# Kernel tuning notes

Hardware: AMD Instinct MI355X
Metric: run time of the kernel (lower is better)

## Reference

```python
import jax, jax.numpy as jnp
import numpy as np

B, L1, L2, DIN, H, DK, DV = 16, 1024, 1024, 1024, 16, 64, 64


def setup_inputs() -> dict:
    key = jax.random.key(0)
    ks = jax.random.split(key, 9)
    s = 1.0 / np.sqrt(DIN)
    return {
        "x": jax.random.normal(ks[0], (B, L1, DIN), dtype=jnp.float32),
        "y": jax.random.normal(ks[1], (B, L2, DIN), dtype=jnp.float32),
        "y_mask": jax.random.randint(ks[2], (B, L2), 0, 2) == 1,  # True => masked
        "Wq": jax.random.normal(ks[3], (DIN, H * DK), dtype=jnp.float32) * s,
        "bq": jnp.zeros((H * DK,), dtype=jnp.float32),
        "Wk": jax.random.normal(ks[4], (DIN, H * DK), dtype=jnp.float32) * s,
        "bk": jnp.zeros((H * DK,), dtype=jnp.float32),
        "Wv": jax.random.normal(ks[5], (DIN, H * DV), dtype=jnp.float32) * s,
        "bv": jnp.zeros((H * DV,), dtype=jnp.float32),
    }


def reference(x, y, y_mask, Wq, bq, Wk, bk, Wv, bv):
    b, l1, _ = x.shape
    l2 = y.shape[1]
    # QKV projections, split into heads: [b, len, H, d]
    q = (x @ Wq + bq).reshape(b, l1, H, DK)
    k = (y @ Wk + bk).reshape(b, l2, H, DK)
    v = (y @ Wv + bv).reshape(b, l2, H, DV)
    # (do_relu=False -> no relu)
    scores = jnp.einsum("bqhd,bkhd->bhqk", q, k) / jnp.sqrt(jnp.float32(DK))
    scores = jnp.where(y_mask[:, None, None, :], -jnp.inf, scores)
    alpha = jax.nn.softmax(scores, axis=-1)  # over len2
    out = jnp.einsum("bhqk,bkhd->bqhd", alpha, v)
    return out.reshape(b, l1, H * DV)
```

## Files before the change

kernel.cpp:

```cpp
#include <hip/hip_runtime.h>
#include <hip/hip_bf16.h>

#define BATCH 16
#define L1D 1024
#define L2D 1024
#define DIN 1024
#define NH 16
#define HD 1024
#define OHD 3072

typedef __attribute__((ext_vector_type(4))) float floatx4;
typedef __attribute__((ext_vector_type(8))) short shortx8;
typedef __attribute__((ext_vector_type(8))) unsigned short ushortx8;

#if __has_builtin(__builtin_amdgcn_exp2f)
#define EXP2(x) __builtin_amdgcn_exp2f(x)
#else
#define EXP2(x) exp2f(x)
#endif

static __device__ __forceinline__ unsigned short f2bf(float f) {
    union { float f; unsigned u; } v; v.f = f;
    unsigned r = v.u + 0x7fff + ((v.u >> 16) & 1);
    return (unsigned short)(r >> 16);
}
static __device__ __forceinline__ unsigned short f2bf_fast(float f) {
    union { float f; unsigned u; } v; v.f = f;
    return (unsigned short)((v.u + 0x8000u) >> 16);
}

#define GLOBAL_AS __attribute__((address_space(1)))
#define LDS_AS __attribute__((address_space(3)))
static __device__ __forceinline__ void gl2lds16(const unsigned short* g, unsigned short* l) {
    __builtin_amdgcn_global_load_lds((const GLOBAL_AS unsigned int*)g,
                                     (LDS_AS unsigned int*)l, 16, 0, 0);
}

#define NCVT 8192
__global__ void prep_kernel(const float* __restrict__ x, const float* __restrict__ y,
                            unsigned short* __restrict__ xb, unsigned short* __restrict__ yb,
                            const int* __restrict__ ym, float* __restrict__ biasf) {
    int bid = blockIdx.x;
    if (bid < 2 * NCVT) {
        const float* in = bid < NCVT ? x : y;
        unsigned short* o = bid < NCVT ? xb : yb;
        int bb = bid < NCVT ? bid : bid - NCVT;
        size_t i = ((size_t)bb * 256 + threadIdx.x) * 8;
        float4 a = *(const float4*)(in + i);
        float4 b = *(const float4*)(in + i + 4);
        ushortx8 v;
        v[0] = f2bf(a.x); v[1] = f2bf(a.y); v[2] = f2bf(a.z); v[3] = f2bf(a.w);
        v[4] = f2bf(b.x); v[5] = f2bf(b.y); v[6] = f2bf(b.z); v[7] = f2bf(b.w);
        *(ushortx8*)(o + i) = v;
    } else {
        int i = (bid - 2 * NCVT) * 256 + threadIdx.x;
        biasf[i] = ym[i] ? -INFINITY : 0.0f;
    }
}

__global__ void wt_kernel(const float* __restrict__ Wq, const float* __restrict__ Wk,
                          const float* __restrict__ Wv, unsigned short* __restrict__ Wt) {
    __shared__ float tile[32][33];
    const float* W = blockIdx.z == 0 ? Wq : (blockIdx.z == 1 ? Wk : Wv);
    unsigned short* dst = Wt + (size_t)blockIdx.z * HD * DIN;
    int bx = blockIdx.x, by = blockIdx.y;
    int tx = threadIdx.x, ty = threadIdx.y;
    for (int i = 0; i < 4; i++)
        tile[ty + i * 8][tx] = W[(size_t)(by * 32 + ty + i * 8) * HD + bx * 32 + tx];
    __syncthreads();
    for (int i = 0; i < 4; i++)
        dst[(size_t)(bx * 32 + ty + i * 8) * DIN + by * 32 + tx] = f2bf(tile[tx][ty + i * 8]);
}

__global__ __launch_bounds__(256, 2) void gemm_kernel(
    const unsigned short* __restrict__ xb, const unsigned short* __restrict__ yb,
    const unsigned short* __restrict__ Wt,
    const float* __restrict__ bq, const float* __restrict__ bk, const float* __restrict__ bvp,
    unsigned short* __restrict__ Out, float qscale)
{
    __shared__ unsigned short As[128 * 32];
    __shared__ unsigned short Bs[128 * 32];
    const int n0 = blockIdx.x * 128;
    const int m0 = blockIdx.y * 128;
    const int sec = n0 >> 10;
    const unsigned short* A = (sec == 0) ? xb : yb;
    const float* bias = (sec == 0) ? bq : (sec == 1 ? bk : bvp);
    const float scale = (sec == 0) ? qscale : 1.0f;

    const int tid = threadIdx.x;
    const int wid = tid >> 6, lane = tid & 63;
    const int c = lane & 15, qd = lane >> 4;
    const int wm = (wid >> 1) * 64, wn = (wid & 1) * 64;

    int f16a = tid, f16b = 256 + tid;
    int rowA = f16a >> 2, scA = ((f16a & 3) ^ ((rowA >> 1) & 3)) * 8;
    int rowB = f16b >> 2, scB = ((f16b & 3) ^ ((rowB >> 1) & 3)) * 8;
    const int swz = (qd ^ ((c >> 1) & 3)) * 8;

    floatx4 acc[4][4] = {};

    for (int k0 = 0; k0 < DIN; k0 += 32) {
        gl2lds16(A  + (size_t)(m0 + rowA) * DIN + k0 + scA, &As[f16a * 8]);
        gl2lds16(Wt + (size_t)(n0 + rowA) * DIN + k0 + scA, &Bs[f16a * 8]);
        gl2lds16(A  + (size_t)(m0 + rowB) * DIN + k0 + scB, &As[f16b * 8]);
        gl2lds16(Wt + (size_t)(n0 + rowB) * DIN + k0 + scB, &Bs[f16b * 8]);
        __syncthreads();

        shortx8 a[4], b[4];
        for (int mt = 0; mt < 4; mt++)
            a[mt] = *(shortx8*)(&As[(wm + mt * 16 + c) * 32 + swz]);
        for (int nt = 0; nt < 4; nt++)
            b[nt] = *(shortx8*)(&Bs[(wn + nt * 16 + c) * 32 + swz]);
        for (int mt = 0; mt < 4; mt++)
            for (int nt = 0; nt < 4; nt++)
                acc[mt][nt] = __builtin_amdgcn_mfma_f32_16x16x32_bf16(
                    a[mt], b[nt], acc[mt][nt], 0, 0, 0);
        __syncthreads();
    }

    for (int nt = 0; nt < 4; nt++) {
        int gn = n0 + wn + nt * 16 + c;
        float bv = bias[gn & 1023];
        for (int mt = 0; mt < 4; mt++)
            for (int r = 0; r < 4; r++) {
                int gm = m0 + wm + mt * 16 + qd * 4 + r;
                Out[(size_t)gm * OHD + gn] = f2bf((acc[mt][nt][r] + bv) * scale);
            }
    }
}

__global__ void vt_kernel(const unsigned short* __restrict__ V,
                          unsigned short* __restrict__ Vt) {
    __shared__ unsigned short t[64][72];
    const int l20 = blockIdx.x * 64;
    const int bh  = blockIdx.y;
    const int b = bh >> 4, h = bh & 15;
    const int tid = threadIdx.x;
    for (int i = 0; i < 2; i++) {
        int idx = i * 256 + tid;
        int row = idx >> 3, col = (idx & 7) * 8;
        *(ushortx8*)(&t[row][col]) =
            *(const ushortx8*)(V + (size_t)(b * L2D + l20 + row) * OHD + h * 64 + col);
    }
    __syncthreads();
    for (int i = 0; i < 2; i++) {
        int idx = i * 256 + tid;
        int dv = idx >> 3, col = (idx & 7) * 8;
        ushortx8 v;
        for (int j = 0; j < 8; j++) v[j] = t[col + j][dv];
        *(ushortx8*)(Vt + (size_t)(bh * 64 + dv) * L2D + l20 + col) = v;
    }
}

__global__ __launch_bounds__(256, 4) void attn_kernel(
    const unsigned short* __restrict__ QK,
    const unsigned short* __restrict__ Vt, const float* __restrict__ biasf,
    float* __restrict__ out)
{
    __shared__ unsigned short Ks[64 * 64];
    __shared__ unsigned short Vs[64 * 64];
    __shared__ unsigned short Ps[4][32 * 72];

    int f = blockIdx.y * gridDim.x + blockIdx.x;
    int bh = (f & 7) * 32 + (f >> 6);
    int q0 = ((f >> 3) & 7) * 128;
    const int b = bh >> 4, h = bh & 15;
    const int tid = threadIdx.x, wid = tid >> 6, lane = tid & 63;
    const int c = lane & 15, qd = lane >> 4;

    shortx8 qf[2][2];
    for (int mt2 = 0; mt2 < 2; mt2++)
        for (int kt = 0; kt < 2; kt++)
            qf[mt2][kt] = *(const shortx8*)(QK +
                (size_t)(b * L1D + q0 + wid * 32 + mt2 * 16 + c) * OHD + h * 64 + kt * 32 + qd * 8);

    floatx4 o[2][4] = {};
    float psum[2][4] = {};

    const unsigned short* Kbase = QK + HD + (size_t)b * L2D * OHD + h * 64;
    const unsigned short* Vbase = Vt + (size_t)bh * 64 * L2D;
    const float* bb = biasf + b * L2D;

    int idxa = tid, idxb = 256 + tid;
    int rowa = idxa >> 3, sca = ((idxa & 7) ^ (rowa & 7)) * 8;
    int rowb = idxb >> 3, scb = ((idxb & 7) ^ (rowb & 7)) * 8;
    const int swz8 = c & 7;

    for (int kv0 = 0; kv0 < L2D; kv0 += 64) {
        gl2lds16(Kbase + (size_t)(kv0 + rowa) * OHD + sca, &Ks[idxa * 8]);
        gl2lds16(Vbase + (size_t)rowa * L2D + kv0 + sca, &Vs[idxa * 8]);
        gl2lds16(Kbase + (size_t)(kv0 + rowb) * OHD + scb, &Ks[idxb * 8]);
        gl2lds16(Vbase + (size_t)rowb * L2D + kv0 + scb, &Vs[idxb * 8]);
        __syncthreads();

        float bv[4];
        for (int nt = 0; nt < 4; nt++) bv[nt] = bb[kv0 + nt * 16 + c];

        for (int mt2 = 0; mt2 < 2; mt2++) {
            for (int nt = 0; nt < 4; nt++) {
                floatx4 z = {};
                for (int kt = 0; kt < 2; kt++) {
                    shortx8 kf = *(shortx8*)(&Ks[(nt * 16 + c) * 64 + ((kt * 4 + qd) ^ swz8) * 8]);
                    z = __builtin_amdgcn_mfma_f32_16x16x32_bf16(qf[mt2][kt], kf, z, 0, 0, 0);
                }
                for (int r = 0; r < 4; r++) {
                    float p = EXP2(z[r] + bv[nt]);
                    psum[mt2][r] += p;
                    Ps[wid][(mt2 * 16 + qd * 4 + r) * 72 + nt * 16 + c] = f2bf_fast(p);
                }
            }
        }
        for (int mt2 = 0; mt2 < 2; mt2++) {
            shortx8 pf[2];
            for (int kt = 0; kt < 2; kt++)
                pf[kt] = *(shortx8*)(&Ps[wid][(mt2 * 16 + c) * 72 + kt * 32 + qd * 8]);
            for (int nt = 0; nt < 4; nt++)
                for (int kt = 0; kt < 2; kt++) {
                    shortx8 vf = *(shortx8*)(&Vs[(nt * 16 + c) * 64 + ((kt * 4 + qd) ^ swz8) * 8]);
                    o[mt2][nt] = __builtin_amdgcn_mfma_f32_16x16x32_bf16(pf[kt], vf, o[mt2][nt], 0, 0, 0);
                }
        }
        __syncthreads();
    }

    for (int mt2 = 0; mt2 < 2; mt2++)
        for (int r = 0; r < 4; r++) {
            float l = psum[mt2][r];
            for (int off = 1; off < 16; off <<= 1)
                l += __shfl_xor(l, off, 64);
            float inv = 1.0f / l;
            size_t rowbase = ((size_t)b * L1D + q0 + wid * 32 + mt2 * 16 + qd * 4 + r) * HD + h * 64;
            for (int nt = 0; nt < 4; nt++)
                out[rowbase + nt * 16 + c] = o[mt2][nt][r] * inv;
        }
}

extern "C" void kernel_launch(void* const* d_in, const int* in_sizes, int n_in,
                              void* d_out, int out_size, void* d_ws, size_t ws_size,
                              hipStream_t stream) {
    const float* x  = (const float*)d_in[0];
    const float* y  = (const float*)d_in[1];
    const int*  ym  = (const int*)d_in[2];
    const float* Wq = (const float*)d_in[3];
    const float* bq = (const float*)d_in[4];
    const float* Wk = (const float*)d_in[5];
    const float* bk = (const float*)d_in[6];
    const float* Wv = (const float*)d_in[7];
    const float* bv = (const float*)d_in[8];
    float* outp = (float*)d_out;

    const size_t M = (size_t)BATCH * L1D;
    const size_t T = M * HD;
    unsigned short* Obuf = (unsigned short*)d_ws;
    unsigned short* xb   = Obuf + M * OHD;
    unsigned short* yb   = xb + T;
    unsigned short* Wt   = yb + T;
    float* biasf         = (float*)(Wt + (size_t)OHD * DIN);

    const float QSCALE = 0.125f * 1.44269504088896340736f;

    prep_kernel<<<2 * NCVT + (BATCH * L2D) / 256, 256, 0, stream>>>(x, y, xb, yb, ym, biasf);
    wt_kernel<<<dim3(HD / 32, DIN / 32, 3), dim3(32, 8), 0, stream>>>(Wq, Wk, Wv, Wt);
    gemm_kernel<<<dim3(OHD / 128, M / 128), 256, 0, stream>>>(xb, yb, Wt, bq, bk, bv, Obuf, QSCALE);
    vt_kernel<<<dim3(L2D / 64, BATCH * NH), 256, 0, stream>>>(Obuf + 2 * HD, xb);
    attn_kernel<<<dim3(L1D / 128, BATCH * NH), 256, 0, stream>>>(Obuf, xb, biasf, outp);
}
```

Baseline: 429.3 us.

## Rewrite QKV projection GEMM with 256x256 tiles and double-buffered LDS pipeline

The projection GEMM moves from 128x128 tiles, 256 threads and a single-buffered K=32 loop to 256x256 tiles, 512 threads and K=64 steps. LDS is double-buffered and global-to-LDS staging is interleaved with MFMA quadrants under explicit waitcnt and barrier control, plus s_setprio around the MFMA bursts. A grid swizzle remaps block indices for L2 locality and bias values are loaded once before the loop. The aim is to hide memory latency and raise reuse per tile; the cost is 128KB of LDS per block, many more barriers, and larger register pressure from the 8x4 accumulator.

```diff
diff --git a/kernel.cpp b/kernel.cpp
--- a/kernel.cpp
+++ b/kernel.cpp
@@ -72,59 +72,163 @@
         dst[(size_t)(bx * 32 + ty + i * 8) * DIN + by * 32 + tx] = f2bf(tile[tx][ty + i * 8]);
 }
 
-__global__ __launch_bounds__(256, 2) void gemm_kernel(
+__global__ __launch_bounds__(512, 2) void gemm_kernel(
     const unsigned short* __restrict__ xb, const unsigned short* __restrict__ yb,
     const unsigned short* __restrict__ Wt,
     const float* __restrict__ bq, const float* __restrict__ bk, const float* __restrict__ bvp,
     unsigned short* __restrict__ Out, float qscale)
 {
-    __shared__ unsigned short As[128 * 32];
-    __shared__ unsigned short Bs[128 * 32];
-    const int n0 = blockIdx.x * 128;
-    const int m0 = blockIdx.y * 128;
+    __shared__ unsigned short As[2][256 * 64];
+    __shared__ unsigned short Bs[2][256 * 64];
+
+    int f = blockIdx.y * gridDim.x + blockIdx.x;
+    int swz = (f & 7) * 96 + (f >> 3);
+    const int n0 = (swz % 12) * 256;
+    const int m0 = (swz / 12) * 256;
     const int sec = n0 >> 10;
-    const unsigned short* A = (sec == 0) ? xb : yb;
+    const unsigned short* Aptr = (sec == 0) ? xb : yb;
     const float* bias = (sec == 0) ? bq : (sec == 1 ? bk : bvp);
     const float scale = (sec == 0) ? qscale : 1.0f;
 
     const int tid = threadIdx.x;
     const int wid = tid >> 6, lane = tid & 63;
     const int c = lane & 15, qd = lane >> 4;
-    const int wm = (wid >> 1) * 64, wn = (wid & 1) * 64;
-
-    int f16a = tid, f16b = 256 + tid;
-    int rowA = f16a >> 2, scA = ((f16a & 3) ^ ((rowA >> 1) & 3)) * 8;
-    int rowB = f16b >> 2, scB = ((f16b & 3) ^ ((rowB >> 1) & 3)) * 8;
-    const int swz = (qd ^ ((c >> 1) & 3)) * 8;
-
-    floatx4 acc[4][4] = {};
-
-    for (int k0 = 0; k0 < DIN; k0 += 32) {
-        gl2lds16(A  + (size_t)(m0 + rowA) * DIN + k0 + scA, &As[f16a * 8]);
-        gl2lds16(Wt + (size_t)(n0 + rowA) * DIN + k0 + scA, &Bs[f16a * 8]);
-        gl2lds16(A  + (size_t)(m0 + rowB) * DIN + k0 + scB, &As[f16b * 8]);
-        gl2lds16(Wt + (size_t)(n0 + rowB) * DIN + k0 + scB, &Bs[f16b * 8]);
-        __syncthreads();
-
-        shortx8 a[4], b[4];
-        for (int mt = 0; mt < 4; mt++)
-            a[mt] = *(shortx8*)(&As[(wm + mt * 16 + c) * 32 + swz]);
-        for (int nt = 0; nt < 4; nt++)
-            b[nt] = *(shortx8*)(&Bs[(wn + nt * 16 + c) * 32 + swz]);
-        for (int mt = 0; mt < 4; mt++)
-            for (int nt = 0; nt < 4; nt++)
-                acc[mt][nt] = __builtin_amdgcn_mfma_f32_16x16x32_bf16(
-                    a[mt], b[nt], acc[mt][nt], 0, 0, 0);
-        __syncthreads();
-    }
-
-    for (int nt = 0; nt < 4; nt++) {
-        int gn = n0 + wn + nt * 16 + c;
-        float bv = bias[gn & 1023];
-        for (int mt = 0; mt < 4; mt++)
+    const int cswz = c & 7;
+    const int R0 = (wid >> 2) * 128;
+    const int C0 = (wid & 3) * 64;
+
+    const int srow = tid >> 3;
+    const int sphys = tid & 7;
+    const int scol = (sphys ^ (srow & 7)) * 8;
+
+    floatx4 acc[8][4] = {};
+    shortx8 a[4][2];
+    shortx8 b0[2][2], b1[2][2];
+
+    auto dsrdA = [&](int mq, const unsigned short* buf) {
+#pragma unroll
+        for (int i = 0; i < 4; i++)
+#pragma unroll
+            for (int kk = 0; kk < 2; kk++)
+                a[i][kk] = *(const shortx8*)&buf[(R0 + mq * 64 + i * 16 + c) * 64 +
+                                                 (((kk * 4 + qd) ^ cswz) * 8)];
+    };
+    auto dsrdB = [&](shortx8 (&bt)[2][2], int nq, const unsigned short* buf) {
+#pragma unroll
+        for (int j = 0; j < 2; j++)
+#pragma unroll
+            for (int kk = 0; kk < 2; kk++)
+                bt[j][kk] = *(const shortx8*)&buf[(C0 + (nq * 2 + j) * 16 + c) * 64 +
+                                                  (((kk * 4 + qd) ^ cswz) * 8)];
+    };
+    auto mfmaQ = [&](int mq, int nq, shortx8 (&bt)[2][2]) {
+        __builtin_amdgcn_s_setprio(1);
+#pragma unroll
+        for (int kk = 0; kk < 2; kk++)
+#pragma unroll
+            for (int i = 0; i < 4; i++)
+#pragma unroll
+                for (int j = 0; j < 2; j++)
+                    acc[mq * 4 + i][nq * 2 + j] = __builtin_amdgcn_mfma_f32_16x16x32_bf16(
+                        a[i][kk], bt[j][kk], acc[mq * 4 + i][nq * 2 + j], 0, 0, 0);
+        __builtin_amdgcn_s_setprio(0);
+    };
+    auto stageA = [&](unsigned short* dst, int h, int kt) {
+        const unsigned short* g = Aptr + (size_t)(m0 + h * 128 + srow) * DIN + kt * 64 + scol;
+        unsigned short* l = dst + (h * 128 + srow) * 64 + sphys * 8;
+        gl2lds16(g, l);
+        gl2lds16(g + (size_t)64 * DIN, l + 64 * 64);
+    };
+    auto stageB = [&](unsigned short* dst, int h, int kt) {
+        const unsigned short* g = Wt + (size_t)(n0 + h * 128 + srow) * DIN + kt * 64 + scol;
+        unsigned short* l = dst + (h * 128 + srow) * 64 + sphys * 8;
+        gl2lds16(g, l);
+        gl2lds16(g + (size_t)64 * DIN, l + 64 * 64);
+    };
+
+    float biasv[4];
+#pragma unroll
+    for (int nf = 0; nf < 4; nf++)
+        biasv[nf] = bias[((n0 & 1023) + C0 + nf * 16 + c) & 1023];
+    asm volatile("s_waitcnt vmcnt(0)" ::: "memory");
+
+    stageB(Bs[0], 0, 0); stageB(Bs[0], 1, 0);
+    stageA(As[0], 0, 0); stageA(As[0], 1, 0);
+    stageB(Bs[1], 0, 1); stageB(Bs[1], 1, 1);
+    asm volatile("s_waitcnt vmcnt(4)" ::: "memory");
+    __builtin_amdgcn_s_barrier();
+
+    for (int it = 0; it < 8; ++it) {
+        const int kt1 = 2 * it + 1;
+        const int ktp = 2 * it + 2;
+        const bool pf = (it < 7);
+
+        dsrdA(0, As[0]); dsrdB(b0, 0, Bs[0]);
+        stageA(As[1], 0, kt1);
+        __builtin_amdgcn_s_barrier();
+        asm volatile("s_waitcnt lgkmcnt(0)" ::: "memory");
+        mfmaQ(0, 0, b0);
+        __builtin_amdgcn_s_barrier();
+
+        dsrdB(b1, 1, Bs[0]);
+        stageA(As[1], 1, kt1);
+        __builtin_amdgcn_s_barrier();
+        asm volatile("s_waitcnt lgkmcnt(0)" ::: "memory");
+        mfmaQ(0, 1, b1);
+        __builtin_amdgcn_s_barrier();
+
+        dsrdA(1, As[0]);
+        if (pf) stageB(Bs[0], 0, ktp);
+        __builtin_amdgcn_s_barrier();
+        asm volatile("s_waitcnt lgkmcnt(0)" ::: "memory");
+        mfmaQ(1, 1, b1);
+        __builtin_amdgcn_s_barrier();
+
+        if (pf) stageB(Bs[0], 1, ktp);
+        __builtin_amdgcn_s_barrier();
+        mfmaQ(1, 0, b0);
+        if (pf) asm volatile("s_waitcnt vmcnt(4)" ::: "memory");
+        else    asm volatile("s_waitcnt vmcnt(0)" ::: "memory");
+        __builtin_amdgcn_s_barrier();
+
+        dsrdA(0, As[1]); dsrdB(b0, 0, Bs[1]);
+        if (pf) stageA(As[0], 0, ktp);
+        __builtin_amdgcn_s_barrier();
+        asm volatile("s_waitcnt lgkmcnt(0)" ::: "memory");
+        mfmaQ(0, 0, b0);
+        __builtin_amdgcn_s_barrier();
+
+        dsrdB(b1, 1, Bs[1]);
+        if (pf) stageA(As[0], 1, ktp);
+        __builtin_amdgcn_s_barrier();
+        asm volatile("s_waitcnt lgkmcnt(0)" ::: "memory");
+        mfmaQ(0, 1, b1);
+        __builtin_amdgcn_s_barrier();
+
+        dsrdA(1, As[1]);
+        if (pf) stageB(Bs[1], 0, ktp + 1);
+        __builtin_amdgcn_s_barrier();
+        asm volatile("s_waitcnt lgkmcnt(0)" ::: "memory");
+        mfmaQ(1, 1, b1);
+        __builtin_amdgcn_s_barrier();
+
+        if (pf) stageB(Bs[1], 1, ktp + 1);
+        __builtin_amdgcn_s_barrier();
+        mfmaQ(1, 0, b0);
+        if (pf) asm volatile("s_waitcnt vmcnt(4)" ::: "memory");
+        __builtin_amdgcn_s_barrier();
+    }
+
+#pragma unroll
+    for (int nf = 0; nf < 4; nf++) {
+        const int gn = n0 + C0 + nf * 16 + c;
+        const float bvv = biasv[nf];
+#pragma unroll
+        for (int mf = 0; mf < 8; mf++)
+#pragma unroll
             for (int r = 0; r < 4; r++) {
-                int gm = m0 + wm + mt * 16 + qd * 4 + r;
-                Out[(size_t)gm * OHD + gn] = f2bf((acc[mt][nt][r] + bv) * scale);
+                const int gm = m0 + R0 + mf * 16 + qd * 4 + r;
+                Out[(size_t)gm * OHD + gn] = f2bf((acc[mf][nf][r] + bvv) * scale);
             }
     }
 }
@@ -261,7 +365,7 @@
 
     prep_kernel<<<2 * NCVT + (BATCH * L2D) / 256, 256, 0, stream>>>(x, y, xb, yb, ym, biasf);
     wt_kernel<<<dim3(HD / 32, DIN / 32, 3), dim3(32, 8), 0, stream>>>(Wq, Wk, Wv, Wt);
-    gemm_kernel<<<dim3(OHD / 128, M / 128), 256, 0, stream>>>(xb, yb, Wt, bq, bk, bv, Obuf, QSCALE);
+    gemm_kernel<<<dim3(OHD / 256, M / 256), 512, 0, stream>>>(xb, yb, Wt, bq, bk, bv, Obuf, QSCALE);
     vt_kernel<<<dim3(L2D / 64, BATCH * NH), 256, 0, stream>>>(Obuf + 2 * HD, xb);
     attn_kernel<<<dim3(L1D / 128, BATCH * NH), 256, 0, stream>>>(Obuf, xb, biasf, outp);
 }
```

Measured after the change: 412.9 us. 1.04x faster.
